# Kernel tuning notes

Measured on AMD Instinct MI355X. Metric: run time of the kernel, lower is better.

The kernel has to match this reference:

```python
import jax, jax.numpy as jnp
import numpy as np

ALPHA = 0.8
TOPK = 9
LOW_BOUND = 0.0
EPS = 1e-10
IOU_EPS = 1e-6


def pairwise_iou(boxes1, boxes2):
    # boxes1 [N,4], boxes2 [G,4] in x1,y1,x2,y2 -> IoU [N,G] (mmdet BboxOverlaps2D)
    area1 = (boxes1[:, 2] - boxes1[:, 0]) * (boxes1[:, 3] - boxes1[:, 1])  # [N]
    area2 = (boxes2[:, 2] - boxes2[:, 0]) * (boxes2[:, 3] - boxes2[:, 1])  # [G]
    lt = jnp.maximum(boxes1[:, None, :2], boxes2[None, :, :2])  # [N,G,2]
    rb = jnp.minimum(boxes1[:, None, 2:], boxes2[None, :, 2:])  # [N,G,2]
    wh = jnp.clip(rb - lt, 0.0)
    inter = wh[..., 0] * wh[..., 1]  # [N,G]
    union = area1[:, None] + area2[None, :] - inter
    return inter / jnp.maximum(union, IOU_EPS)


def setup_inputs() -> dict:
    key = jax.random.key(0)
    k1, k2, k3, k4, k5, k6, k7 = jax.random.split(key, 7)
    N, G, C = 65536, 256, 80
    IMG = 1024.0
    points = jax.random.uniform(k1, (N, 2), dtype=jnp.float32) * IMG  # (cy, cx)
    p_xy1 = jax.random.uniform(k2, (N, 2), dtype=jnp.float32) * (IMG - 96.0)
    p_wh = jax.random.uniform(k3, (N, 2), dtype=jnp.float32) * 95.0 + 1.0
    bbox_preds = jnp.concatenate([p_xy1, p_xy1 + p_wh], axis=1)  # valid x1y1x2y2
    g_xy1 = jax.random.uniform(k4, (G, 2), dtype=jnp.float32) * (IMG - 256.0)
    g_wh = jax.random.uniform(k5, (G, 2), dtype=jnp.float32) * 255.0 + 1.0
    gt_bboxes = jnp.concatenate([g_xy1, g_xy1 + g_wh], axis=1)
    cls_scores = jax.random.normal(k6, (N, C), dtype=jnp.float32)
    gt_labels = jax.random.randint(k7, (G,), 0, C)
    return {"points": points, "cls_scores": cls_scores, "bbox_preds": bbox_preds,
            "gt_bboxes": gt_bboxes, "gt_labels": gt_labels}


def reference(points, cls_scores, bbox_preds, gt_bboxes, gt_labels):
    num_points = points.shape[0]
    num_gt = gt_bboxes.shape[0]
    overlaps = pairwise_iou(bbox_preds, gt_bboxes)  # [N,G]
    cls_cost = jax.nn.sigmoid(cls_scores[:, gt_labels])  # [N,G]
    overlaps = cls_cost ** (1.0 - ALPHA) * overlaps ** ALPHA
    # top-k points per GT (torch: overlaps.topk(k, dim=0))
    _, topk_idxs = jax.lax.top_k(overlaps.T, TOPK)  # [G,K]
    candidate_idxs = topk_idxs.T  # [K,G]
    cp = jnp.transpose(points[candidate_idxs], (1, 0, 2))  # [G,K,2] (cy,cx)
    # mle_2d_gaussian_2: per-GT MLE Gaussian over candidate points
    miu = cp.mean(axis=1, keepdims=True)  # [G,1,2]
    diff = cp - miu  # [G,K,2]
    sigma = jnp.einsum('gki,gkj->gij', diff, diff) / TOPK  # [G,2,2]
    a, b = sigma[:, 0, 0], sigma[:, 0, 1]
    c, d = sigma[:, 1, 0], sigma[:, 1, 1]
    det = a * d - b * c  # [G]
    inv = jnp.stack([jnp.stack([d, -b], axis=-1),
                     jnp.stack([-c, a], axis=-1)], axis=-2) / (det + EPS)[:, None, None]
    maha = jnp.einsum('gki,gij,gkj->gk', diff, inv, diff)  # [G,K]
    candidate_w = jnp.exp(-0.5 * maha).T  # [K,G]
    # center-inside-gt validity, evaluated only at candidate points
    cy, cx = cp[:, :, 0], cp[:, :, 1]  # [G,K]
    gx1, gy1, gx2, gy2 = (gt_bboxes[:, i][:, None] for i in range(4))  # [G,1]
    valid = ((cx - gx1 > EPS) & (cy - gy1 > EPS) &
             (gx2 - cx > EPS) & (gy2 - cy > EPS)).T  # [K,G]
    wv = candidate_w * valid.astype(candidate_w.dtype)
    # scatter per-GT weights to points, then max over GTs == scatter-max
    w = jnp.zeros((num_points,), dtype=cls_scores.dtype)
    w = w.at[candidate_idxs.reshape(-1)].max(wv.reshape(-1))
    w = jnp.where(w < LOW_BOUND, jnp.zeros_like(w), w)
    return w
```

## Files before the change

### kernel.cpp

```cpp
#include <hip/hip_runtime.h>
#include <hip/hip_bf16.h>
#include <math.h>

#define NPTS   65536
#define NGT    256
#define NCLS   80
#define TOPK   9
#define GSLICE 32
#define NPB    256
#define NXB    (NPTS / NPB)
#define SCAP   64

__device__ inline unsigned long long pack_key(float L, unsigned idx) {
    unsigned u   = __float_as_uint(L);
    unsigned k32 = (u & 0x80000000u) ? ~u : (u | 0x80000000u);
    return ((unsigned long long)k32 << 32) | (unsigned)(~idx);
}

__device__ inline unsigned long long umax64(unsigned long long a,
                                            unsigned long long b) {
    return a > b ? a : b;
}

__global__ __launch_bounds__(256) void filter_kernel(
    const float* __restrict__ preds,
    const float* __restrict__ gtb,
    const int*   __restrict__ glab,
    const float* __restrict__ cls,
    unsigned short* __restrict__ counts,
    unsigned long long* __restrict__ bucket,
    float* __restrict__ w)
{
    __shared__ unsigned lcnt[GSLICE];
    __shared__ int      glabs[GSLICE];
    __shared__ unsigned long long stage[GSLICE][SCAP];

    const int t   = threadIdx.x;
    const int xb  = blockIdx.x;
    const int g0  = blockIdx.y * GSLICE;
    const int pt  = xb * NPB + t;
    const int bid = blockIdx.y * NXB + xb;

    if (t < GSLICE) {
        lcnt[t]  = 0u;
        glabs[t] = glab[g0 + t];
    }
    if (t < 32) w[bid * 32 + t] = 0.0f;

    float4 pb = ((const float4*)preds)[pt];
    float parea = (pb.z - pb.x) * (pb.w - pb.y);
    __syncthreads();

    for (int gi = 0; gi < GSLICE; ++gi) {
        const float4 g4 = ((const float4*)gtb)[g0 + gi];
        float ix1 = fmaxf(pb.x, g4.x), iy1 = fmaxf(pb.y, g4.y);
        float ix2 = fminf(pb.z, g4.z), iy2 = fminf(pb.w, g4.w);
        float iw  = fmaxf(ix2 - ix1, 0.0f);
        float ih  = fmaxf(iy2 - iy1, 0.0f);
        float inter = iw * ih;
        if (inter > 0.0f) {
            float garea = (g4.z - g4.x) * (g4.w - g4.y);
            float uni = fmaxf(parea + garea - inter, 1e-6f);
            float iou = inter / uni;
            unsigned long long entry =
                ((unsigned long long)__float_as_uint(iou) << 32) |
                (unsigned)(~(unsigned)pt);
            unsigned slot = atomicAdd(&lcnt[gi], 1u);
            if (slot < SCAP) stage[gi][slot] = entry;
        }
    }
    __syncthreads();

    if (t < GSLICE) {
        unsigned c = lcnt[t];
        if (c > SCAP) c = SCAP;
        lcnt[t] = c;
        counts[(size_t)(g0 + t) * NXB + xb] = (unsigned short)c;
    }
    __syncthreads();

    const float E1 = 1.0f - 0.8f;
#pragma unroll
    for (int k = 0; k < 8; k += 4) {
        unsigned long long e[4];
        bool  vld[4];
        int   gi[4];
        float x[4];
#pragma unroll
        for (int j = 0; j < 4; ++j) {
            int i = (k + j) * 256 + t;
            gi[j] = i >> 6;
            int sl = i & (SCAP - 1);
            e[j]   = stage[gi[j]][sl];
            vld[j] = sl < (int)lcnt[gi[j]];
        }
#pragma unroll
        for (int j = 0; j < 4; ++j) {
            if (vld[j]) {
                unsigned p = ~(unsigned)(e[j] & 0xFFFFFFFFu);
                x[j] = cls[(size_t)p * NCLS + glabs[gi[j]]];
            }
        }
#pragma unroll
        for (int j = 0; j < 4; ++j) {
            if (vld[j]) {
                float iou = __uint_as_float((unsigned)(e[j] >> 32));
                float s   = 1.0f / (1.0f + expf(-x[j]));
                float L   = E1 * log2f(s) + 0.8f * log2f(iou);
                unsigned u   = __float_as_uint(L);
                unsigned k32 = (u & 0x80000000u) ? ~u : (u | 0x80000000u);
                int i = (k + j) * 256 + t;
                bucket[((size_t)(g0 + gi[j]) * NXB + xb) * SCAP + (i & (SCAP - 1))]
                    = ((unsigned long long)k32 << 32) | (e[j] & 0xFFFFFFFFu);
            }
        }
    }
}

__global__ __launch_bounds__(1024) void select_kernel(
    const unsigned short*     __restrict__ counts,
    const unsigned long long* __restrict__ bucket,
    const float* __restrict__ pts,
    const float* __restrict__ gtb,
    float* __restrict__ w)
{
    const int g    = blockIdx.x;
    const int t    = threadIdx.x;
    const int lane = t & 63;
    const int wid  = t >> 6;

    __shared__ unsigned short scnt[NXB];
    __shared__ unsigned long long wmax[16];
    __shared__ unsigned long long winner_s;
    __shared__ unsigned tidx[TOPK];
    __shared__ float ppy[TOPK], ppx[TOPK];

    if (t < NXB) scnt[t] = counts[(size_t)g * NXB + t];
    __syncthreads();

    unsigned long long e[17];
#pragma unroll
    for (int k = 0; k < 16; k += 4) {
#pragma unroll
        for (int j = 0; j < 4; ++j) {
            int i = (k + j) * 1024 + t;
            unsigned long long v = bucket[(size_t)g * (NXB * SCAP) + i];
            bool vld = (i & (SCAP - 1)) < (int)scnt[i >> 6];
            e[k + j] = vld ? v : 0ULL;
        }
    }
    e[16] = (t < TOPK) ? pack_key(-INFINITY, (unsigned)t) : 0ULL;

    unsigned long long mymax = 0ULL;
#pragma unroll
    for (int j = 0; j < 17; ++j) mymax = umax64(mymax, e[j]);

    for (int r = 0; r < TOPK; ++r) {
        unsigned long long m = mymax;
#pragma unroll
        for (int off = 1; off < 64; off <<= 1)
            m = umax64(m, (unsigned long long)__shfl_xor(m, off));
        if (lane == 0) wmax[wid] = m;
        __syncthreads();
        if (t == 0) {
            unsigned long long win = wmax[0];
#pragma unroll
            for (int wv = 1; wv < 16; ++wv) win = umax64(win, wmax[wv]);
            winner_s = win;
            tidx[r]  = ~(unsigned)(win & 0xFFFFFFFFu);
        }
        __syncthreads();
        unsigned long long win = winner_s;
        if (mymax == win) {
#pragma unroll
            for (int j = 0; j < 17; ++j)
                if (e[j] == win) e[j] = 0ULL;
            mymax = 0ULL;
#pragma unroll
            for (int j = 0; j < 17; ++j) mymax = umax64(mymax, e[j]);
        }
    }
    __syncthreads();

    if (t < TOPK) {
        unsigned pi = tidx[t];
        ppy[t] = pts[2 * (size_t)pi];
        ppx[t] = pts[2 * (size_t)pi + 1];
    }
    __syncthreads();

    if (t == 0) {
        float4 g4 = ((const float4*)gtb)[g];
        float m0 = 0.0f, m1 = 0.0f;
#pragma unroll
        for (int k = 0; k < TOPK; ++k) { m0 += ppy[k]; m1 += ppx[k]; }
        m0 /= (float)TOPK; m1 /= (float)TOPK;

        float d0[TOPK], d1[TOPK];
        float a = 0.0f, bb = 0.0f, dd = 0.0f;
#pragma unroll
        for (int k = 0; k < TOPK; ++k) {
            d0[k] = ppy[k] - m0;
            d1[k] = ppx[k] - m1;
            a  += d0[k] * d0[k];
            bb += d0[k] * d1[k];
            dd += d1[k] * d1[k];
        }
        a /= (float)TOPK; bb /= (float)TOPK; dd /= (float)TOPK;
        float det  = a * dd - bb * bb;
        float rinv = 1.0f / (det + 1e-10f);

#pragma unroll
        for (int k = 0; k < TOPK; ++k) {
            float q = d0[k] * (dd * d0[k] - bb * d1[k])
                    + d1[k] * (a  * d1[k] - bb * d0[k]);
            float maha = q * rinv;
            float wt = expf(-0.5f * maha);
            bool valid = (ppx[k] - g4.x > 1e-10f) && (ppy[k] - g4.y > 1e-10f) &&
                         (g4.z - ppx[k] > 1e-10f) && (g4.w - ppy[k] > 1e-10f);
            float wv = valid ? wt : 0.0f;
            atomicMax((int*)&w[tidx[k]], __float_as_int(wv));
        }
    }
}

extern "C" void kernel_launch(void* const* d_in, const int* in_sizes, int n_in,
                              void* d_out, int out_size, void* d_ws, size_t ws_size,
                              hipStream_t stream) {
    const float* points  = (const float*)d_in[0];
    const float* cls     = (const float*)d_in[1];
    const float* preds   = (const float*)d_in[2];
    const float* gtb     = (const float*)d_in[3];
    const int*   glab    = (const int*)d_in[4];
    float* w = (float*)d_out;

    char* ws = (char*)d_ws;
    unsigned long long* bucket = (unsigned long long*)ws;
    size_t off = (size_t)NGT * NXB * SCAP * sizeof(unsigned long long);
    unsigned short* counts = (unsigned short*)(ws + off);

    filter_kernel<<<dim3(NXB, NGT / GSLICE), 256, 0, stream>>>(
        preds, gtb, glab, cls, counts, bucket, w);
    select_kernel<<<NGT, 1024, 0, stream>>>(counts, bucket, points, gtb, w);
}
```

Baseline: 112.8 us.

## Split per-GT top-k selection into two-stage wave-local partial selects

Replaces the single 1024-thread-per-GT select kernel with two stages. The first runs 4 blocks per GT, each wave computing a local top-9 with shuffles only, and writes partial candidates. The second merges the 144 partials per GT in one wave and computes the Gaussian weights. This removes the two block-wide barriers per selection round and raises parallelism, at the cost of an extra launch and a small intermediate buffer.

```diff
diff --git a/kernel.cpp b/kernel.cpp
--- a/kernel.cpp
+++ b/kernel.cpp
@@ -10,6 +10,8 @@
 #define NPB    256
 #define NXB    (NPTS / NPB)
 #define SCAP   64
+#define NSUB   4
+#define NWV    16
 
 __device__ inline unsigned long long pack_key(float L, unsigned idx) {
     unsigned u   = __float_as_uint(L);
@@ -20,6 +22,13 @@
 __device__ inline unsigned long long umax64(unsigned long long a,
                                             unsigned long long b) {
     return a > b ? a : b;
+}
+
+__device__ inline unsigned long long wave_max64(unsigned long long m) {
+#pragma unroll
+    for (int off = 1; off < 64; off <<= 1)
+        m = umax64(m, (unsigned long long)__shfl_xor((long long)m, off));
+    return m;
 }
 
 __global__ __launch_bounds__(256) void filter_kernel(
@@ -117,73 +126,97 @@
     }
 }
 
-__global__ __launch_bounds__(1024) void select_kernel(
+__global__ __launch_bounds__(256) void select1_kernel(
     const unsigned short*     __restrict__ counts,
     const unsigned long long* __restrict__ bucket,
+    unsigned long long*       __restrict__ partial)
+{
+    const int g    = blockIdx.x;
+    const int sub  = blockIdx.y;
+    const int t    = threadIdx.x;
+    const int lane = t & 63;
+    const int wv   = t >> 6;
+
+    const unsigned long long* src =
+        bucket + (size_t)g * (NXB * SCAP) + (size_t)sub * 4096;
+    const unsigned short* cnt = counts + (size_t)g * NXB + sub * 64;
+
+    unsigned long long e[16];
+#pragma unroll
+    for (int k = 0; k < 16; k += 4) {
+        unsigned long long v[4];
+#pragma unroll
+        for (int j = 0; j < 4; ++j) v[j] = src[(k + j) * 256 + t];
+#pragma unroll
+        for (int j = 0; j < 4; ++j) {
+            int c = (int)cnt[(k + j) * 4 + wv];
+            e[k + j] = (lane < c) ? v[j] : 0ULL;
+        }
+    }
+    unsigned long long mymax = 0ULL;
+#pragma unroll
+    for (int j = 0; j < 16; ++j) mymax = umax64(mymax, e[j]);
+
+    unsigned long long out[TOPK];
+#pragma unroll
+    for (int r = 0; r < TOPK; ++r) {
+        unsigned long long m = wave_max64(mymax);
+        out[r] = m;
+        if (m != 0ULL && mymax == m) {
+#pragma unroll
+            for (int j = 0; j < 16; ++j) if (e[j] == m) e[j] = 0ULL;
+            mymax = 0ULL;
+#pragma unroll
+            for (int j = 0; j < 16; ++j) mymax = umax64(mymax, e[j]);
+        }
+    }
+    if (lane == 0) {
+        unsigned long long* dst =
+            partial + ((size_t)g * NWV + (size_t)(sub * 4 + wv)) * TOPK;
+#pragma unroll
+        for (int r = 0; r < TOPK; ++r) dst[r] = out[r];
+    }
+}
+
+__global__ __launch_bounds__(64) void select2_kernel(
+    const unsigned long long* __restrict__ partial,
     const float* __restrict__ pts,
     const float* __restrict__ gtb,
     float* __restrict__ w)
 {
-    const int g    = blockIdx.x;
-    const int t    = threadIdx.x;
-    const int lane = t & 63;
-    const int wid  = t >> 6;
-
-    __shared__ unsigned short scnt[NXB];
-    __shared__ unsigned long long wmax[16];
-    __shared__ unsigned long long winner_s;
-    __shared__ unsigned tidx[TOPK];
+    const int g = blockIdx.x;
+    const int t = threadIdx.x;
+
     __shared__ float ppy[TOPK], ppx[TOPK];
-
-    if (t < NXB) scnt[t] = counts[(size_t)g * NXB + t];
-    __syncthreads();
-
-    unsigned long long e[17];
-#pragma unroll
-    for (int k = 0; k < 16; k += 4) {
-#pragma unroll
-        for (int j = 0; j < 4; ++j) {
-            int i = (k + j) * 1024 + t;
-            unsigned long long v = bucket[(size_t)g * (NXB * SCAP) + i];
-            bool vld = (i & (SCAP - 1)) < (int)scnt[i >> 6];
-            e[k + j] = vld ? v : 0ULL;
-        }
-    }
-    e[16] = (t < TOPK) ? pack_key(-INFINITY, (unsigned)t) : 0ULL;
+    __shared__ unsigned tidx_s[TOPK];
+
+    const unsigned long long* src = partial + (size_t)g * (NWV * TOPK);
+    unsigned long long e[4];
+    e[0] = src[t];
+    e[1] = src[64 + t];
+    e[2] = (t < NWV * TOPK - 128) ? src[128 + t] : 0ULL;
+    e[3] = (t < TOPK) ? pack_key(-INFINITY, (unsigned)t) : 0ULL;
 
     unsigned long long mymax = 0ULL;
 #pragma unroll
-    for (int j = 0; j < 17; ++j) mymax = umax64(mymax, e[j]);
-
+    for (int j = 0; j < 4; ++j) mymax = umax64(mymax, e[j]);
+
+#pragma unroll
     for (int r = 0; r < TOPK; ++r) {
-        unsigned long long m = mymax;
-#pragma unroll
-        for (int off = 1; off < 64; off <<= 1)
-            m = umax64(m, (unsigned long long)__shfl_xor(m, off));
-        if (lane == 0) wmax[wid] = m;
-        __syncthreads();
-        if (t == 0) {
-            unsigned long long win = wmax[0];
-#pragma unroll
-            for (int wv = 1; wv < 16; ++wv) win = umax64(win, wmax[wv]);
-            winner_s = win;
-            tidx[r]  = ~(unsigned)(win & 0xFFFFFFFFu);
-        }
-        __syncthreads();
-        unsigned long long win = winner_s;
-        if (mymax == win) {
-#pragma unroll
-            for (int j = 0; j < 17; ++j)
-                if (e[j] == win) e[j] = 0ULL;
+        unsigned long long m = wave_max64(mymax);
+        if (t == 0) tidx_s[r] = ~(unsigned)(m & 0xFFFFFFFFu);
+        if (mymax == m) {
+#pragma unroll
+            for (int j = 0; j < 4; ++j) if (e[j] == m) e[j] = 0ULL;
             mymax = 0ULL;
 #pragma unroll
-            for (int j = 0; j < 17; ++j) mymax = umax64(mymax, e[j]);
+            for (int j = 0; j < 4; ++j) mymax = umax64(mymax, e[j]);
         }
     }
     __syncthreads();
 
     if (t < TOPK) {
-        unsigned pi = tidx[t];
+        unsigned pi = tidx_s[t];
         ppy[t] = pts[2 * (size_t)pi];
         ppx[t] = pts[2 * (size_t)pi + 1];
     }
@@ -219,7 +252,7 @@
             bool valid = (ppx[k] - g4.x > 1e-10f) && (ppy[k] - g4.y > 1e-10f) &&
                          (g4.z - ppx[k] > 1e-10f) && (g4.w - ppy[k] > 1e-10f);
             float wv = valid ? wt : 0.0f;
-            atomicMax((int*)&w[tidx[k]], __float_as_int(wv));
+            atomicMax((int*)&w[tidx_s[k]], __float_as_int(wv));
         }
     }
 }
@@ -238,8 +271,11 @@
     unsigned long long* bucket = (unsigned long long*)ws;
     size_t off = (size_t)NGT * NXB * SCAP * sizeof(unsigned long long);
     unsigned short* counts = (unsigned short*)(ws + off);
+    off += (size_t)NGT * NXB * sizeof(unsigned short);
+    unsigned long long* partial = (unsigned long long*)(ws + off);
 
     filter_kernel<<<dim3(NXB, NGT / GSLICE), 256, 0, stream>>>(
         preds, gtb, glab, cls, counts, bucket, w);
-    select_kernel<<<NGT, 1024, 0, stream>>>(counts, bucket, points, gtb, w);
-}
+    select1_kernel<<<dim3(NGT, NSUB), 256, 0, stream>>>(counts, bucket, partial);
+    select2_kernel<<<NGT, 64, 0, stream>>>(partial, points, gtb, w);
+}
```

Result: slower. 132.4 us (+17.4%).

## Replace block-wide top-k rounds with per-wave top-k then single-wave merge

Applied to the files above, without the earlier changes.

The select kernel used to run nine rounds of block-wide argmax, each with two __syncthreads and a serial reduction by thread 0. Now each wave computes its own local top-9 with shuffle reductions only, writes them to shared memory, and wave 0 merges the 144 candidates into the final top-9. Bucket loads are also remapped so each wave reads a contiguous 1024-entry range, which makes the validity count lookup uniform across the wave. This removes 18 block barriers per GT, at the cost of a second small selection pass.

```diff
diff --git a/kernel.cpp b/kernel.cpp
--- a/kernel.cpp
+++ b/kernel.cpp
@@ -20,6 +20,13 @@
 __device__ inline unsigned long long umax64(unsigned long long a,
                                             unsigned long long b) {
     return a > b ? a : b;
+}
+
+__device__ inline unsigned long long wave_max64(unsigned long long m) {
+#pragma unroll
+    for (int off = 1; off < 64; off <<= 1)
+        m = umax64(m, (unsigned long long)__shfl_xor(m, off));
+    return m;
 }
 
 __global__ __launch_bounds__(256) void filter_kernel(
@@ -130,54 +137,68 @@
     const int wid  = t >> 6;
 
     __shared__ unsigned short scnt[NXB];
-    __shared__ unsigned long long wmax[16];
-    __shared__ unsigned long long winner_s;
+    __shared__ unsigned long long wl[16 * TOPK];
     __shared__ unsigned tidx[TOPK];
     __shared__ float ppy[TOPK], ppx[TOPK];
 
     if (t < NXB) scnt[t] = counts[(size_t)g * NXB + t];
     __syncthreads();
 
-    unsigned long long e[17];
+    const unsigned long long* src =
+        bucket + (size_t)g * (NXB * SCAP) + (size_t)wid * 1024;
+
+    unsigned long long e[16];
 #pragma unroll
     for (int k = 0; k < 16; k += 4) {
-#pragma unroll
-        for (int j = 0; j < 4; ++j) {
-            int i = (k + j) * 1024 + t;
-            unsigned long long v = bucket[(size_t)g * (NXB * SCAP) + i];
-            bool vld = (i & (SCAP - 1)) < (int)scnt[i >> 6];
-            e[k + j] = vld ? v : 0ULL;
-        }
-    }
-    e[16] = (t < TOPK) ? pack_key(-INFINITY, (unsigned)t) : 0ULL;
-
+        unsigned long long v[4];
+#pragma unroll
+        for (int j = 0; j < 4; ++j) v[j] = src[(k + j) * 64 + lane];
+#pragma unroll
+        for (int j = 0; j < 4; ++j) {
+            int c = (int)scnt[wid * 16 + k + j];
+            e[k + j] = (lane < c) ? v[j] : 0ULL;
+        }
+    }
     unsigned long long mymax = 0ULL;
 #pragma unroll
-    for (int j = 0; j < 17; ++j) mymax = umax64(mymax, e[j]);
-
+    for (int j = 0; j < 16; ++j) mymax = umax64(mymax, e[j]);
+
+#pragma unroll
     for (int r = 0; r < TOPK; ++r) {
-        unsigned long long m = mymax;
-#pragma unroll
-        for (int off = 1; off < 64; off <<= 1)
-            m = umax64(m, (unsigned long long)__shfl_xor(m, off));
-        if (lane == 0) wmax[wid] = m;
-        __syncthreads();
-        if (t == 0) {
-            unsigned long long win = wmax[0];
-#pragma unroll
-            for (int wv = 1; wv < 16; ++wv) win = umax64(win, wmax[wv]);
-            winner_s = win;
-            tidx[r]  = ~(unsigned)(win & 0xFFFFFFFFu);
-        }
-        __syncthreads();
-        unsigned long long win = winner_s;
-        if (mymax == win) {
-#pragma unroll
-            for (int j = 0; j < 17; ++j)
-                if (e[j] == win) e[j] = 0ULL;
+        unsigned long long m = wave_max64(mymax);
+        if (lane == 0) wl[wid * TOPK + r] = m;
+        if (m != 0ULL && mymax == m) {
+#pragma unroll
+            for (int j = 0; j < 16; ++j) if (e[j] == m) e[j] = 0ULL;
             mymax = 0ULL;
 #pragma unroll
-            for (int j = 0; j < 17; ++j) mymax = umax64(mymax, e[j]);
+            for (int j = 0; j < 16; ++j) mymax = umax64(mymax, e[j]);
+        }
+    }
+    __syncthreads();
+
+    if (wid == 0) {
+        unsigned long long f[4];
+        f[0] = wl[lane];
+        f[1] = wl[64 + lane];
+        f[2] = (lane < 16) ? wl[128 + lane] : 0ULL;
+        f[3] = (lane < TOPK) ? pack_key(-INFINITY, (unsigned)lane) : 0ULL;
+
+        unsigned long long mx = 0ULL;
+#pragma unroll
+        for (int j = 0; j < 4; ++j) mx = umax64(mx, f[j]);
+
+#pragma unroll
+        for (int r = 0; r < TOPK; ++r) {
+            unsigned long long m = wave_max64(mx);
+            if (lane == 0) tidx[r] = ~(unsigned)(m & 0xFFFFFFFFu);
+            if (mx == m) {
+#pragma unroll
+                for (int j = 0; j < 4; ++j) if (f[j] == m) f[j] = 0ULL;
+                mx = 0ULL;
+#pragma unroll
+                for (int j = 0; j < 4; ++j) mx = umax64(mx, f[j]);
+            }
         }
     }
     __syncthreads();
```

Result: no change. 114.6 us (+1.5%).
